# Performance work log

Measured on AMD Instinct MI355X. Metric: run time of the kernel, lower is better.

The kernel has to match this reference:

```python
import jax, jax.numpy as jnp
import numpy as np

NEG = -9e15
EPS = 1e-5

def setup_inputs() -> dict:
    key = jax.random.key(0)
    k1, k2, k3, k4 = jax.random.split(key, 4)
    B, S, D = 4, 2048, 1024
    q = jax.random.normal(k1, (B, S, D), dtype=jnp.float32)
    k = jax.random.normal(k2, (B, S, D), dtype=jnp.float32)
    v = jax.random.normal(k3, (B, S, D), dtype=jnp.float32)
    mask = jax.random.randint(k4, (B, S, S), 0, 2, dtype=jnp.int32)
    gamma = jnp.ones((D,), dtype=jnp.float32)
    beta = jnp.zeros((D,), dtype=jnp.float32)
    return {"q": q, "k": k, "v": v, "mask": mask, "gamma": gamma, "beta": beta}

def reference(q, k, v, mask, gamma, beta):
    d_k = q.shape[-1]
    # scaled dot-product attention: [B,S,S] logits materialized as in original
    logits = jnp.einsum('bsd,btd->bst', q, k) / jnp.sqrt(jnp.asarray(d_k, q.dtype))
    logits = jnp.where(mask == 0, jnp.asarray(NEG, logits.dtype), logits)
    attn = jax.nn.softmax(logits, axis=-1)
    x = jnp.einsum('bst,btd->bsd', attn, v)
    # dropout is identity at inference; LayerNorm over last dim
    mu = jnp.mean(x, axis=-1, keepdims=True)
    var = jnp.mean(jnp.square(x - mu), axis=-1, keepdims=True)
    xhat = (x - mu) * jax.lax.rsqrt(var + EPS)
    return xhat * gamma + beta
```

## Files before the change

kernel.cpp:

```cpp
#include <hip/hip_runtime.h>
#include <hip/hip_bf16.h>

typedef unsigned short u16;
typedef unsigned long long u64;
typedef __attribute__((ext_vector_type(8))) short bf16x8;
typedef __attribute__((ext_vector_type(4))) float f32x4;
typedef __attribute__((ext_vector_type(4))) float float4v;
typedef __attribute__((ext_vector_type(4))) short short4v;
typedef __attribute__((ext_vector_type(4))) int int4v;
typedef __attribute__((ext_vector_type(4))) unsigned long long u64x4;

#define BB 4
#define SS 2048
#define DD 1024

__device__ __forceinline__ u16 f2bf(float x){
    unsigned u = __float_as_uint(x);
    return (u16)((u + 0x7fffu + ((u >> 16) & 1u)) >> 16);
}

#define GLD16(g, l) __builtin_amdgcn_global_load_lds( \
    (const __attribute__((address_space(1))) unsigned int*)(g), \
    (__attribute__((address_space(3))) unsigned int*)(l), 16, 0, 0)

#define SCHED0() __builtin_amdgcn_sched_barrier(0)
#define PH_PRE()  SCHED0(); __builtin_amdgcn_s_barrier(); SCHED0(); __builtin_amdgcn_s_setprio(1)
#define PH_POST() __builtin_amdgcn_s_setprio(0); SCHED0(); __builtin_amdgcn_s_barrier(); SCHED0()

__global__ __launch_bounds__(256) void prep_kernel(
    const float* __restrict__ q, const float* __restrict__ k,
    const float* __restrict__ v, const int* __restrict__ mask,
    u16* __restrict__ Qb, u16* __restrict__ Kb, u16* __restrict__ Vt,
    u64* __restrict__ mbits64, float* __restrict__ rowsum)
{
    const int bid = blockIdx.x;
    const int tid = threadIdx.x;

    if (bid < 4096){
        const float* in = (bid < 2048) ? q : k;
        u16* out = (bid < 2048) ? Qb : Kb;
        const float scale = (bid < 2048) ? 0.03125f : 1.0f;
        const int sb = bid & 2047;
#pragma unroll
        for (int kk = 0; kk < 4; ++kk){
            int i = sb * 1024 + kk * 256 + tid;
            float4v val = ((const float4v*)in)[i];
            short4v o;
            o[0] = (short)f2bf(val[0] * scale); o[1] = (short)f2bf(val[1] * scale);
            o[2] = (short)f2bf(val[2] * scale); o[3] = (short)f2bf(val[3] * scale);
            ((short4v*)out)[i] = o;
        }
    } else if (bid < 6144){
        __shared__ float tile[64][65];
        const int sb = bid - 4096;
        const int b  = sb >> 9;
        const int r  = sb & 511;
        const int s0 = (r >> 4) << 6;
        const int d0 = (r & 15) << 6;
        const int tx = tid & 15;
        const int ty = tid >> 4;
#pragma unroll
        for (int kk = 0; kk < 4; ++kk){
            const float* p = v + ((size_t)(b * SS + s0 + ty + 16 * kk) * DD) + d0 + tx * 4;
            float4v val = *(const float4v*)p;
            tile[ty + 16 * kk][tx * 4 + 0] = val[0];
            tile[ty + 16 * kk][tx * 4 + 1] = val[1];
            tile[ty + 16 * kk][tx * 4 + 2] = val[2];
            tile[ty + 16 * kk][tx * 4 + 3] = val[3];
        }
        __syncthreads();
#pragma unroll
        for (int kk = 0; kk < 4; ++kk){
            int dy = ty + 16 * kk;
            short4v o;
            o[0] = (short)f2bf(tile[tx * 4 + 0][dy]);
            o[1] = (short)f2bf(tile[tx * 4 + 1][dy]);
            o[2] = (short)f2bf(tile[tx * 4 + 2][dy]);
            o[3] = (short)f2bf(tile[tx * 4 + 3][dy]);
            *(short4v*)&Vt[((size_t)(b * DD + d0 + dy) * SS) + s0 + tx * 4] = o;
        }
    } else if (bid < 8192){
        const int sb = bid - 6144;
        const int tt = sb * 256 + tid;
        const int lane = tid & 63;
#pragma unroll
        for (int j = 0; j < 8; ++j){
            const int idx = j * 524288 + tt;
            int4v mm = ((const int4v*)mask)[idx];
            u64 b0 = __ballot(mm[0] != 0);
            u64 b1 = __ballot(mm[1] != 0);
            u64 b2 = __ballot(mm[2] != 0);
            u64 b3 = __ballot(mm[3] != 0);
            const int gw = idx >> 6;
            if (lane < 4){
                u64 w = (lane == 0) ? b0 : (lane == 1) ? b1 : (lane == 2) ? b2 : b3;
                mbits64[(size_t)gw * 4 + lane] = w;
            }
        }
    } else {
        rowsum[(bid - 8192) * 256 + tid] = 0.f;
    }
}

__global__ __launch_bounds__(256, 2) void qk_kernel(
    const u16* __restrict__ Qb, const u16* __restrict__ Kb,
    const u64* __restrict__ mbits64, u16* __restrict__ P,
    float* __restrict__ rowsum)
{
    __shared__ __align__(16) u16 Qs[2][128 * 64];
    __shared__ __align__(16) u16 Ks[2][128 * 64];

    const int swz = ((blockIdx.x & 7) << 7) + (blockIdx.x >> 3);
    const int b   = swz >> 8;
    const int bx  = (swz >> 4) & 15;
    const int by  = swz & 15;
    const int row0 = bx << 7, col0 = by << 7;

    const int tid = threadIdx.x;
    const int wid = tid >> 6, lane = tid & 63;
    const int l16 = lane & 15, g4 = lane >> 4;
    const int wq = wid >> 1, wk = wid & 1;

    const int sr   = tid >> 3;
    const int scol = ((tid & 7) ^ (sr & 7)) << 3;
    const u16* gA = Qb + (size_t)(b * SS + row0 + sr) * DD + scol;
    const u16* gB = Kb + (size_t)(b * SS + col0 + sr) * DD + scol;
    char* const lA0 = (char*)Qs[0] + tid * 16;
    char* const lB0 = (char*)Ks[0] + tid * 16;
    char* const lA1 = (char*)Qs[1] + tid * 16;
    char* const lB1 = (char*)Ks[1] + tid * 16;

    const int qRow = (wq * 64 + l16) << 7;
    const int kRow = (wk * 64 + l16) << 7;
    const int cx0  = (g4 << 4) ^ ((l16 & 7) << 4);

    f32x4 acc[4][4];
    const f32x4 z4 = {0.f, 0.f, 0.f, 0.f};
#pragma unroll
    for (int i = 0; i < 4; ++i)
#pragma unroll
        for (int j = 0; j < 4; ++j) acc[i][j] = z4;

#define STAGE_QK(kt, la, lb) { \
    const u16* ga_ = gA + (kt) * 64; \
    const u16* gb_ = gB + (kt) * 64; \
    GLD16(ga_,            (la)); \
    GLD16(ga_ + 32 * DD,  (la) + 4096); \
    GLD16(ga_ + 64 * DD,  (la) + 8192); \
    GLD16(ga_ + 96 * DD,  (la) + 12288); \
    GLD16(gb_,            (lb)); \
    GLD16(gb_ + 32 * DD,  (lb) + 4096); \
    GLD16(gb_ + 64 * DD,  (lb) + 8192); \
    GLD16(gb_ + 96 * DD,  (lb) + 12288); }

#define LDQ4(Qb_, kx) { \
    const char* p_ = (const char*)(Qb_) + qRow + ((kx) ? (cx0 ^ 64) : cx0); \
    fq0 = *(const bf16x8*)(p_); \
    fq1 = *(const bf16x8*)(p_ + 2048); \
    fq2 = *(const bf16x8*)(p_ + 4096); \
    fq3 = *(const bf16x8*)(p_ + 6144); }

#define LDK2(Kb_, mh, kx) { \
    const char* p_ = (const char*)(Kb_) + kRow + (mh) * 4096 + ((kx) ? (cx0 ^ 64) : cx0); \
    fk0 = *(const bf16x8*)(p_); \
    fk1 = *(const bf16x8*)(p_ + 2048); }

#define MKROW(mi, fk) \
    acc[mi][0] = __builtin_amdgcn_mfma_f32_16x16x32_bf16(fk, fq0, acc[mi][0],0,0,0); \
    acc[mi][1] = __builtin_amdgcn_mfma_f32_16x16x32_bf16(fk, fq1, acc[mi][1],0,0,0); \
    acc[mi][2] = __builtin_amdgcn_mfma_f32_16x16x32_bf16(fk, fq2, acc[mi][2],0,0,0); \
    acc[mi][3] = __builtin_amdgcn_mfma_f32_16x16x32_bf16(fk, fq3, acc[mi][3],0,0,0);

    STAGE_QK(0, lA0, lB0);
    STAGE_QK(1, lA1, lB1);
    asm volatile("s_waitcnt vmcnt(8)" ::: "memory");
    SCHED0(); __builtin_amdgcn_s_barrier(); SCHED0();

#pragma unroll 1
    for (int it = 0; it < 8; ++it){
        bf16x8 fq0, fq1, fq2, fq3, fk0, fk1;
        LDK2(Ks[0], 0, 0); LDQ4(Qs[0], 0);
        PH_PRE(); MKROW(0,fk0) MKROW(1,fk1) PH_POST();
        LDK2(Ks[0], 1, 0);
        PH_PRE(); MKROW(2,fk0) MKROW(3,fk1) PH_POST();
        LDK2(Ks[0], 0, 1); LDQ4(Qs[0], 1);
        PH_PRE(); MKROW(0,fk0) MKROW(1,fk1) PH_POST();
        LDK2(Ks[0], 1, 1);
        PH_PRE(); MKROW(2,fk0) MKROW(3,fk1) PH_POST();
        if (it < 7){
            STAGE_QK(2*it+2, lA0, lB0);
            asm volatile("s_waitcnt vmcnt(8)" ::: "memory");
        } else {
            asm volatile("s_waitcnt vmcnt(0)" ::: "memory");
        }
        SCHED0(); __builtin_amdgcn_s_barrier(); SCHED0();
        LDK2(Ks[1], 0, 0); LDQ4(Qs[1], 0);
        PH_PRE(); MKROW(0,fk0) MKROW(1,fk1) PH_POST();
        LDK2(Ks[1], 1, 0);
        PH_PRE(); MKROW(2,fk0) MKROW(3,fk1) PH_POST();
        LDK2(Ks[1], 0, 1); LDQ4(Qs[1], 1);
        PH_PRE(); MKROW(0,fk0) MKROW(1,fk1) PH_POST();
        LDK2(Ks[1], 1, 1);
        PH_PRE(); MKROW(2,fk0) MKROW(3,fk1) PH_POST();
        if (it < 7){
            STAGE_QK(2*it+3, lA1, lB1);
            asm volatile("s_waitcnt vmcnt(8)" ::: "memory");
            SCHED0(); __builtin_amdgcn_s_barrier(); SCHED0();
        }
    }
#undef STAGE_QK
#undef LDQ4
#undef LDK2
#undef MKROW

    const int m = (by << 1) | wk;
    const int shbase = ((m & 3) << 4) + g4;
#pragma unroll
    for (int nq = 0; nq < 4; ++nq){
        const int grow = row0 + wq * 64 + nq * 16 + l16;
        const size_t rbase = (size_t)(b * SS + grow) * SS;
        u64x4 w = *(const u64x4*)&mbits64[((size_t)(b * SS + grow) * 8 + (m >> 2)) * 4];
        float rs = 0.f;
#pragma unroll
        for (int mk = 0; mk < 4; ++mk){
            const int sh = shbase + (mk << 2);
            const int gcolb = col0 + wk * 64 + mk * 16 + g4 * 4;
            float e0 = ((w[0] >> sh) & 1ull) ? __expf(acc[mk][nq][0]) : 0.f;
            float e1 = ((w[1] >> sh) & 1ull) ? __expf(acc[mk][nq][1]) : 0.f;
            float e2 = ((w[2] >> sh) & 1ull) ? __expf(acc[mk][nq][2]) : 0.f;
            float e3 = ((w[3] >> sh) & 1ull) ? __expf(acc[mk][nq][3]) : 0.f;
            short4v pp;
            pp[0] = (short)f2bf(e0); pp[1] = (short)f2bf(e1);
            pp[2] = (short)f2bf(e2); pp[3] = (short)f2bf(e3);
            *(short4v*)&P[rbase + gcolb] = pp;
            rs += (e0 + e1) + (e2 + e3);
        }
        rs += __shfl_xor(rs, 16);
        rs += __shfl_xor(rs, 32);
        if (g4 == 0) atomicAdd(&rowsum[b * SS + grow], rs);
    }
}

__global__ __launch_bounds__(512, 2) void pv_kernel(
    const u16* __restrict__ P, const u16* __restrict__ Vt,
    const float* __restrict__ rowsum, u16* __restrict__ Xn)
{
    __shared__ __align__(16) u16 As[2][128 * 64];
    __shared__ __align__(16) u16 Bs[2][256 * 64];

    const int swz = ((blockIdx.x & 7) << 5) + (blockIdx.x >> 3);
    const int b   = swz >> 6;
    const int bx  = (swz >> 2) & 15;
    const int by  = swz & 3;
    const int row0 = bx << 7, col0 = by << 8;

    const int tid = threadIdx.x;
    const int wid = tid >> 6, lane = tid & 63;
    const int l16 = lane & 15, g4 = lane >> 4;
    const int wr = wid >> 2, wc = wid & 3;

    const int sr   = tid >> 3;
    const int scol = ((tid & 7) ^ (sr & 7)) << 3;
    const u16* gA = P  + (size_t)(b * SS + row0 + sr) * SS + scol;
    const u16* gB = Vt + (size_t)(b * DD + col0 + sr) * SS + scol;
    char* const lA0 = (char*)As[0] + tid * 16;
    char* const lB0 = (char*)Bs[0] + tid * 16;
    char* const lA1 = (char*)As[1] + tid * 16;
    char* const lB1 = (char*)Bs[1] + tid * 16;

    const int aRow = (wr * 64 + l16) << 7;
    const int bRow = (wc * 64 + l16) << 7;
    const int cx0  = (g4 << 4) ^ ((l16 & 7) << 4);

    f32x4 acc[4][4];
    const f32x4 z4 = {0.f, 0.f, 0.f, 0.f};
#pragma unroll
    for (int i = 0; i < 4; ++i)
#pragma unroll
        for (int j = 0; j < 4; ++j) acc[i][j] = z4;

#define STAGE_PV(kt, la, lb) { \
    const u16* ga_ = gA + (kt) * 64; \
    const u16* gb_ = gB + (kt) * 64; \
    GLD16(ga_,            (la)); \
    GLD16(ga_ +  64 * SS, (la) + 8192); \
    GLD16(gb_,            (lb)); \
    GLD16(gb_ +  64 * SS, (lb) + 8192); \
    GLD16(gb_ + 128 * SS, (lb) + 16384); \
    GLD16(gb_ + 192 * SS, (lb) + 24576); }

#define LDA2(Ab_, mh, kx) { \
    const char* p_ = (const char*)(Ab_) + aRow + (mh) * 4096 + ((kx) ? (cx0 ^ 64) : cx0); \
    fa0 = *(const bf16x8*)(p_); \
    fa1 = *(const bf16x8*)(p_ + 2048); }

#define LDB4(Bb_, kx) { \
    const char* p_ = (const char*)(Bb_) + bRow + ((kx) ? (cx0 ^ 64) : cx0); \
    fb0 = *(const bf16x8*)(p_); \
    fb1 = *(const bf16x8*)(p_ + 2048); \
    fb2 = *(const bf16x8*)(p_ + 4096); \
    fb3 = *(const bf16x8*)(p_ + 6144); }

#define MROWP(mi, fa) \
    acc[mi][0] = __builtin_amdgcn_mfma_f32_16x16x32_bf16(fa, fb0, acc[mi][0],0,0,0); \
    acc[mi][1] = __builtin_amdgcn_mfma_f32_16x16x32_bf16(fa, fb1, acc[mi][1],0,0,0); \
    acc[mi][2] = __builtin_amdgcn_mfma_f32_16x16x32_bf16(fa, fb2, acc[mi][2],0,0,0); \
    acc[mi][3] = __builtin_amdgcn_mfma_f32_16x16x32_bf16(fa, fb3, acc[mi][3],0,0,0);

    STAGE_PV(0, lA0, lB0);
    STAGE_PV(1, lA1, lB1);
    asm volatile("s_waitcnt vmcnt(6)" ::: "memory");
    SCHED0(); __builtin_amdgcn_s_barrier(); SCHED0();

#pragma unroll 1
    for (int it = 0; it < 16; ++it){
        bf16x8 fa0, fa1, fb0, fb1, fb2, fb3;
        LDA2(As[0], 0, 0); LDB4(Bs[0], 0);
        PH_PRE(); MROWP(0,fa0) MROWP(1,fa1) PH_POST();
        LDA2(As[0], 1, 0);
        PH_PRE(); MROWP(2,fa0) MROWP(3,fa1) PH_POST();
        LDA2(As[0], 0, 1); LDB4(Bs[0], 1);
        PH_PRE(); MROWP(0,fa0) MROWP(1,fa1) PH_POST();
        LDA2(As[0], 1, 1);
        PH_PRE(); MROWP(2,fa0) MROWP(3,fa1) PH_POST();
        if (it < 15){
            STAGE_PV(2*it+2, lA0, lB0);
            asm volatile("s_waitcnt vmcnt(6)" ::: "memory");
        } else {
            asm volatile("s_waitcnt vmcnt(0)" ::: "memory");
        }
        SCHED0(); __builtin_amdgcn_s_barrier(); SCHED0();
        LDA2(As[1], 0, 0); LDB4(Bs[1], 0);
        PH_PRE(); MROWP(0,fa0) MROWP(1,fa1) PH_POST();
        LDA2(As[1], 1, 0);
        PH_PRE(); MROWP(2,fa0) MROWP(3,fa1) PH_POST();
        LDA2(As[1], 0, 1); LDB4(Bs[1], 1);
        PH_PRE(); MROWP(0,fa0) MROWP(1,fa1) PH_POST();
        LDA2(As[1], 1, 1);
        PH_PRE(); MROWP(2,fa0) MROWP(3,fa1) PH_POST();
        if (it < 15){
            STAGE_PV(2*it+3, lA1, lB1);
            asm volatile("s_waitcnt vmcnt(6)" ::: "memory");
            SCHED0(); __builtin_amdgcn_s_barrier(); SCHED0();
        }
    }
#undef STAGE_PV
#undef LDA2
#undef LDB4
#undef MROWP

#pragma unroll
    for (int m = 0; m < 4; ++m){
        float inv[4];
#pragma unroll
        for (int r = 0; r < 4; ++r)
            inv[r] = 1.f / rowsum[b * SS + row0 + wr * 64 + m * 16 + g4 * 4 + r];
#pragma unroll
        for (int n = 0; n < 4; ++n){
            const int gcol = col0 + wc * 64 + n * 16 + l16;
#pragma unroll
            for (int r = 0; r < 4; ++r){
                const int grow = row0 + wr * 64 + m * 16 + g4 * 4 + r;
                Xn[(size_t)(b * SS + grow) * DD + gcol] = f2bf(acc[m][n][r] * inv[r]);
            }
        }
    }
}

__global__ __launch_bounds__(256) void ln_kernel(
    const u16* __restrict__ Xn, const float* __restrict__ gamma,
    const float* __restrict__ beta, float* __restrict__ out)
{
    __shared__ float red[2][4];
    const int row = blockIdx.x;
    const int t = threadIdx.x;
    short4v xv = *(const short4v*)&Xn[(size_t)row * DD + t * 4];
    float x[4];
#pragma unroll
    for (int j = 0; j < 4; ++j)
        x[j] = __uint_as_float(((unsigned)(u16)xv[j]) << 16);
    float s  = x[0] + x[1] + x[2] + x[3];
    float sq = x[0]*x[0] + x[1]*x[1] + x[2]*x[2] + x[3]*x[3];
#pragma unroll
    for (int d = 1; d < 64; d <<= 1){ s += __shfl_xor(s, d); sq += __shfl_xor(sq, d); }
    const int wv = t >> 6;
    if ((t & 63) == 0){ red[0][wv] = s; red[1][wv] = sq; }
    __syncthreads();
    float S  = red[0][0] + red[0][1] + red[0][2] + red[0][3];
    float Sq = red[1][0] + red[1][1] + red[1][2] + red[1][3];
    float mu = S * (1.f / 1024.f);
    float var = Sq * (1.f / 1024.f) - mu * mu;
    float rstd = rsqrtf(var + 1e-5f);
    float4v g  = *(const float4v*)&gamma[t * 4];
    float4v be = *(const float4v*)&beta[t * 4];
    float4v o;
#pragma unroll
    for (int j = 0; j < 4; ++j) o[j] = (x[j] - mu) * rstd * g[j] + be[j];
    *(float4v*)&out[(size_t)row * DD + t * 4] = o;
}

extern "C" void kernel_launch(void* const* d_in, const int* in_sizes, int n_in,
                              void* d_out, int out_size, void* d_ws, size_t ws_size,
                              hipStream_t stream) {
    const float* q     = (const float*)d_in[0];
    const float* k     = (const float*)d_in[1];
    const float* v     = (const float*)d_in[2];
    const int*   mask  = (const int*)d_in[3];
    const float* gamma = (const float*)d_in[4];
    const float* beta  = (const float*)d_in[5];
    float* out = (float*)d_out;

    u16* Qb = (u16*)d_ws;
    u16* Kb = Qb + (size_t)BB * SS * DD;
    u16* Vt = Kb + (size_t)BB * SS * DD;
    u16* P  = Vt + (size_t)BB * SS * DD;
    u16* Xn = P  + (size_t)BB * SS * SS;
    float* rowsum = (float*)(Xn + (size_t)BB * SS * DD);
    u64* mbits64 = (u64*)Xn;

    prep_kernel<<<8224, 256, 0, stream>>>(q, k, v, mask, Qb, Kb, Vt, mbits64, rowsum);
    qk_kernel<<<1024, 256, 0, stream>>>(Qb, Kb, mbits64, P, rowsum);
    pv_kernel<<<256, 512, 0, stream>>>(P, Vt, rowsum, Xn);
    ln_kernel<<<BB * SS, 256, 0, stream>>>(Xn, gamma, beta, out);
}
```

Before: 141.1 us.

## Fuse Q/K fp32-to-bf16 conversion into the QK GEMM load path

```diff
diff --git a/kernel.cpp b/kernel.cpp
--- a/kernel.cpp
+++ b/kernel.cpp
@@ -8,6 +8,7 @@
 typedef __attribute__((ext_vector_type(4))) float float4v;
 typedef __attribute__((ext_vector_type(4))) short short4v;
 typedef __attribute__((ext_vector_type(4))) int int4v;
+typedef __attribute__((ext_vector_type(4))) unsigned int u32x4;
 typedef __attribute__((ext_vector_type(4))) unsigned long long u64x4;
 
 #define BB 4
@@ -19,6 +20,12 @@
     return (u16)((u + 0x7fffu + ((u >> 16) & 1u)) >> 16);
 }
 
+__device__ __forceinline__ unsigned cvtpk(float lo, float hi){
+    unsigned r;
+    asm("v_cvt_pk_bf16_f32 %0, %1, %2" : "=v"(r) : "v"(lo), "v"(hi));
+    return r;
+}
+
 #define GLD16(g, l) __builtin_amdgcn_global_load_lds( \
     (const __attribute__((address_space(1))) unsigned int*)(g), \
     (__attribute__((address_space(3))) unsigned int*)(l), 16, 0, 0)
@@ -28,31 +35,15 @@
 #define PH_POST() __builtin_amdgcn_s_setprio(0); SCHED0(); __builtin_amdgcn_s_barrier(); SCHED0()
 
 __global__ __launch_bounds__(256) void prep_kernel(
-    const float* __restrict__ q, const float* __restrict__ k,
     const float* __restrict__ v, const int* __restrict__ mask,
-    u16* __restrict__ Qb, u16* __restrict__ Kb, u16* __restrict__ Vt,
-    u64* __restrict__ mbits64, float* __restrict__ rowsum)
+    u16* __restrict__ Vt, u64* __restrict__ mbits64, float* __restrict__ rowsum)
 {
     const int bid = blockIdx.x;
     const int tid = threadIdx.x;
 
-    if (bid < 4096){
-        const float* in = (bid < 2048) ? q : k;
-        u16* out = (bid < 2048) ? Qb : Kb;
-        const float scale = (bid < 2048) ? 0.03125f : 1.0f;
-        const int sb = bid & 2047;
-#pragma unroll
-        for (int kk = 0; kk < 4; ++kk){
-            int i = sb * 1024 + kk * 256 + tid;
-            float4v val = ((const float4v*)in)[i];
-            short4v o;
-            o[0] = (short)f2bf(val[0] * scale); o[1] = (short)f2bf(val[1] * scale);
-            o[2] = (short)f2bf(val[2] * scale); o[3] = (short)f2bf(val[3] * scale);
-            ((short4v*)out)[i] = o;
-        }
-    } else if (bid < 6144){
+    if (bid < 2048){
         __shared__ float tile[64][65];
-        const int sb = bid - 4096;
+        const int sb = bid;
         const int b  = sb >> 9;
         const int r  = sb & 511;
         const int s0 = (r >> 4) << 6;
@@ -79,8 +70,8 @@
             o[3] = (short)f2bf(tile[tx * 4 + 3][dy]);
             *(short4v*)&Vt[((size_t)(b * DD + d0 + dy) * SS) + s0 + tx * 4] = o;
         }
-    } else if (bid < 8192){
-        const int sb = bid - 6144;
+    } else if (bid < 4096){
+        const int sb = bid - 2048;
         const int tt = sb * 256 + tid;
         const int lane = tid & 63;
 #pragma unroll
@@ -98,12 +89,12 @@
             }
         }
     } else {
-        rowsum[(bid - 8192) * 256 + tid] = 0.f;
+        rowsum[(bid - 4096) * 256 + tid] = 0.f;
     }
 }
 
 __global__ __launch_bounds__(256, 2) void qk_kernel(
-    const u16* __restrict__ Qb, const u16* __restrict__ Kb,
+    const float* __restrict__ qf, const float* __restrict__ kf,
     const u64* __restrict__ mbits64, u16* __restrict__ P,
     float* __restrict__ rowsum)
 {
@@ -123,12 +114,8 @@
 
     const int sr   = tid >> 3;
     const int scol = ((tid & 7) ^ (sr & 7)) << 3;
-    const u16* gA = Qb + (size_t)(b * SS + row0 + sr) * DD + scol;
-    const u16* gB = Kb + (size_t)(b * SS + col0 + sr) * DD + scol;
-    char* const lA0 = (char*)Qs[0] + tid * 16;
-    char* const lB0 = (char*)Ks[0] + tid * 16;
-    char* const lA1 = (char*)Qs[1] + tid * 16;
-    char* const lB1 = (char*)Ks[1] + tid * 16;
+    const float* qbase = qf + (size_t)(b * SS + row0 + sr) * DD + scol;
+    const float* kbase = kf + (size_t)(b * SS + col0 + sr) * DD + scol;
 
     const int qRow = (wq * 64 + l16) << 7;
     const int kRow = (wk * 64 + l16) << 7;
@@ -141,17 +128,32 @@
 #pragma unroll
         for (int j = 0; j < 4; ++j) acc[i][j] = z4;
 
-#define STAGE_QK(kt, la, lb) { \
-    const u16* ga_ = gA + (kt) * 64; \
-    const u16* gb_ = gB + (kt) * 64; \
-    GLD16(ga_,            (la)); \
-    GLD16(ga_ + 32 * DD,  (la) + 4096); \
-    GLD16(ga_ + 64 * DD,  (la) + 8192); \
-    GLD16(ga_ + 96 * DD,  (la) + 12288); \
-    GLD16(gb_,            (lb)); \
-    GLD16(gb_ + 32 * DD,  (lb) + 4096); \
-    GLD16(gb_ + 64 * DD,  (lb) + 8192); \
-    GLD16(gb_ + 96 * DD,  (lb) + 12288); }
+    float4v ra0, ra1, ra2, ra3, ra4, ra5, ra6, ra7;
+    float4v rb0, rb1, rb2, rb3, rb4, rb5, rb6, rb7;
+
+#define LOADF(kt) { \
+    const float* ga_ = qbase + (kt) * 64; \
+    const float* gb_ = kbase + (kt) * 64; \
+    ra0 = *(const float4v*)(ga_);               ra1 = *(const float4v*)(ga_ + 4); \
+    ra2 = *(const float4v*)(ga_ + 32 * DD);     ra3 = *(const float4v*)(ga_ + 32 * DD + 4); \
+    ra4 = *(const float4v*)(ga_ + 64 * DD);     ra5 = *(const float4v*)(ga_ + 64 * DD + 4); \
+    ra6 = *(const float4v*)(ga_ + 96 * DD);     ra7 = *(const float4v*)(ga_ + 96 * DD + 4); \
+    rb0 = *(const float4v*)(gb_);               rb1 = *(const float4v*)(gb_ + 4); \
+    rb2 = *(const float4v*)(gb_ + 32 * DD);     rb3 = *(const float4v*)(gb_ + 32 * DD + 4); \
+    rb4 = *(const float4v*)(gb_ + 64 * DD);     rb5 = *(const float4v*)(gb_ + 64 * DD + 4); \
+    rb6 = *(const float4v*)(gb_ + 96 * DD);     rb7 = *(const float4v*)(gb_ + 96 * DD + 4); }
+
+#define CVTW1(dst, off, x0, x1) { \
+    u32x4 w_; \
+    w_[0] = cvtpk(x0[0], x0[1]); w_[1] = cvtpk(x0[2], x0[3]); \
+    w_[2] = cvtpk(x1[0], x1[1]); w_[3] = cvtpk(x1[2], x1[3]); \
+    *(u32x4*)((char*)(dst) + tid * 16 + (off)) = w_; }
+
+#define CVTW(qb_, kb_) { \
+    CVTW1(qb_, 0,     ra0, ra1); CVTW1(qb_, 4096,  ra2, ra3); \
+    CVTW1(qb_, 8192,  ra4, ra5); CVTW1(qb_, 12288, ra6, ra7); \
+    CVTW1(kb_, 0,     rb0, rb1); CVTW1(kb_, 4096,  rb2, rb3); \
+    CVTW1(kb_, 8192,  rb4, rb5); CVTW1(kb_, 12288, rb6, rb7); }
 
 #define LDQ4(Qb_, kx) { \
     const char* p_ = (const char*)(Qb_) + qRow + ((kx) ? (cx0 ^ 64) : cx0); \
@@ -171,44 +173,38 @@
     acc[mi][2] = __builtin_amdgcn_mfma_f32_16x16x32_bf16(fk, fq2, acc[mi][2],0,0,0); \
     acc[mi][3] = __builtin_amdgcn_mfma_f32_16x16x32_bf16(fk, fq3, acc[mi][3],0,0,0);
 
-    STAGE_QK(0, lA0, lB0);
-    STAGE_QK(1, lA1, lB1);
-    asm volatile("s_waitcnt vmcnt(8)" ::: "memory");
+    LOADF(0);
+    asm volatile("s_waitcnt vmcnt(0)" ::: "memory");
+    CVTW(Qs[0], Ks[0]);
+    LOADF(1);
+    asm volatile("s_waitcnt lgkmcnt(0)" ::: "memory");
     SCHED0(); __builtin_amdgcn_s_barrier(); SCHED0();
 
 #pragma unroll 1
-    for (int it = 0; it < 8; ++it){
+    for (int it = 0; it < 16; ++it){
+        const int cur = it & 1;
+        u16* Qc = Qs[cur]; u16* Kc = Ks[cur];
         bf16x8 fq0, fq1, fq2, fq3, fk0, fk1;
-        LDK2(Ks[0], 0, 0); LDQ4(Qs[0], 0);
+        LDK2(Kc, 0, 0); LDQ4(Qc, 0);
         PH_PRE(); MKROW(0,fk0) MKROW(1,fk1) PH_POST();
-        LDK2(Ks[0], 1, 0);
+        LDK2(Kc, 1, 0);
         PH_PRE(); MKROW(2,fk0) MKROW(3,fk1) PH_POST();
-        LDK2(Ks[0], 0, 1); LDQ4(Qs[0], 1);
+        LDK2(Kc, 0, 1); LDQ4(Qc, 1);
         PH_PRE(); MKROW(0,fk0) MKROW(1,fk1) PH_POST();
-        LDK2(Ks[0], 1, 1);
+        LDK2(Kc, 1, 1);
         PH_PRE(); MKROW(2,fk0) MKROW(3,fk1) PH_POST();
-        if (it < 7){
-            STAGE_QK(2*it+2, lA0, lB0);
-            asm volatile("s_waitcnt vmcnt(8)" ::: "memory");
-        } else {
+        if (it < 15){
             asm volatile("s_waitcnt vmcnt(0)" ::: "memory");
-        }
-        SCHED0(); __builtin_amdgcn_s_barrier(); SCHED0();
-        LDK2(Ks[1], 0, 0); LDQ4(Qs[1], 0);
-        PH_PRE(); MKROW(0,fk0) MKROW(1,fk1) PH_POST();
-        LDK2(Ks[1], 1, 0);
-        PH_PRE(); MKROW(2,fk0) MKROW(3,fk1) PH_POST();
-        LDK2(Ks[1], 0, 1); LDQ4(Qs[1], 1);
-        PH_PRE(); MKROW(0,fk0) MKROW(1,fk1) PH_POST();
-        LDK2(Ks[1], 1, 1);
-        PH_PRE(); MKROW(2,fk0) MKROW(3,fk1) PH_POST();
-        if (it < 7){
-            STAGE_QK(2*it+3, lA1, lB1);
-            asm volatile("s_waitcnt vmcnt(8)" ::: "memory");
+            SCHED0();
+            CVTW(Qs[cur ^ 1], Ks[cur ^ 1]);
+            if (it < 14) LOADF(it + 2);
+            asm volatile("s_waitcnt lgkmcnt(0)" ::: "memory");
             SCHED0(); __builtin_amdgcn_s_barrier(); SCHED0();
         }
     }
-#undef STAGE_QK
+#undef LOADF
+#undef CVTW
+#undef CVTW1
 #undef LDQ4
 #undef LDK2
 #undef MKROW
@@ -225,10 +221,10 @@
         for (int mk = 0; mk < 4; ++mk){
             const int sh = shbase + (mk << 2);
             const int gcolb = col0 + wk * 64 + mk * 16 + g4 * 4;
-            float e0 = ((w[0] >> sh) & 1ull) ? __expf(acc[mk][nq][0]) : 0.f;
-            float e1 = ((w[1] >> sh) & 1ull) ? __expf(acc[mk][nq][1]) : 0.f;
-            float e2 = ((w[2] >> sh) & 1ull) ? __expf(acc[mk][nq][2]) : 0.f;
-            float e3 = ((w[3] >> sh) & 1ull) ? __expf(acc[mk][nq][3]) : 0.f;
+            float e0 = ((w[0] >> sh) & 1ull) ? __expf(acc[mk][nq][0] * 0.03125f) : 0.f;
+            float e1 = ((w[1] >> sh) & 1ull) ? __expf(acc[mk][nq][1] * 0.03125f) : 0.f;
+            float e2 = ((w[2] >> sh) & 1ull) ? __expf(acc[mk][nq][2] * 0.03125f) : 0.f;
+            float e3 = ((w[3] >> sh) & 1ull) ? __expf(acc[mk][nq][3] * 0.03125f) : 0.f;
             short4v pp;
             pp[0] = (short)f2bf(e0); pp[1] = (short)f2bf(e1);
             pp[2] = (short)f2bf(e2); pp[3] = (short)f2bf(e3);
@@ -410,16 +406,14 @@
     const float* beta  = (const float*)d_in[5];
     float* out = (float*)d_out;
 
-    u16* Qb = (u16*)d_ws;
-    u16* Kb = Qb + (size_t)BB * SS * DD;
-    u16* Vt = Kb + (size_t)BB * SS * DD;
+    u16* Vt = (u16*)d_ws;
     u16* P  = Vt + (size_t)BB * SS * DD;
     u16* Xn = P  + (size_t)BB * SS * SS;
     float* rowsum = (float*)(Xn + (size_t)BB * SS * DD);
     u64* mbits64 = (u64*)Xn;
 
-    prep_kernel<<<8224, 256, 0, stream>>>(q, k, v, mask, Qb, Kb, Vt, mbits64, rowsum);
-    qk_kernel<<<1024, 256, 0, stream>>>(Qb, Kb, mbits64, P, rowsum);
+    prep_kernel<<<4128, 256, 0, stream>>>(v, mask, Vt, mbits64, rowsum);
+    qk_kernel<<<1024, 256, 0, stream>>>(q, k, mbits64, P, rowsum);
     pv_kernel<<<256, 512, 0, stream>>>(P, Vt, rowsum, Xn);
     ln_kernel<<<BB * SS, 256, 0, stream>>>(Xn, gamma, beta, out);
 }
```

Result: no change. 142.6 us (+1.0%).
